# Performance work log

Hardware: AMD Instinct MI355X
Metric: run time of the kernel (lower is better)

The kernel has to match this reference:

```python
import jax, jax.numpy as jnp
import numpy as np
from jax import lax

B, LATENT, SEQ, HID, OUT = 4096, 128, 512, 32, 64


def setup_inputs() -> dict:
    key = jax.random.key(0)
    ks = jax.random.split(key, 9)
    s = 1.0 / np.sqrt(HID)  # PyTorch-style init scale
    f32 = jnp.float32
    return {
        "z": jax.random.normal(ks[0], (B, LATENT), f32),
        "init_W": jax.random.uniform(ks[1], (HID, LATENT), f32, -s, s),
        "init_b": jax.random.uniform(ks[2], (HID,), f32, -s, s),
        "W_ih": jax.random.uniform(ks[3], (4 * HID, HID), f32, -s, s),
        "W_hh": jax.random.uniform(ks[4], (4 * HID, HID), f32, -s, s),
        "b_ih": jax.random.uniform(ks[5], (4 * HID,), f32, -s, s),
        "b_hh": jax.random.uniform(ks[6], (4 * HID,), f32, -s, s),
        "out_W": jax.random.uniform(ks[7], (OUT, HID), f32, -s, s),
        "out_b": jax.random.uniform(ks[8], (OUT,), f32, -s, s),
    }


def reference(z, init_W, init_b, W_ih, W_hh, b_ih, b_hh, out_W, out_b):
    # init_fc: z -> h0 (num_layers=1); cell starts at zero
    h0 = z @ init_W.T + init_b  # [B, H]
    c0 = jnp.zeros_like(h0)

    # x_in is all zeros, so the input-to-hidden term is a constant bias;
    # compute it once (keeps W_ih in the graph, matmul with zeros == 0).
    x_zero = jnp.zeros((z.shape[0], W_ih.shape[1]), z.dtype)
    gate_const = x_zero @ W_ih.T + b_ih + b_hh  # [B, 4H]

    def step(carry, _):
        h, c = carry
        gates = h @ W_hh.T + gate_const  # [B, 4H], PyTorch gate order i,f,g,o
        i, f, g, o = jnp.split(gates, 4, axis=-1)
        i = jax.nn.sigmoid(i)
        f = jax.nn.sigmoid(f)
        g = jnp.tanh(g)
        o = jax.nn.sigmoid(o)
        c = f * c + i * g
        h = o * jnp.tanh(c)
        return (h, c), h

    _, hs = lax.scan(step, (h0, c0), None, length=SEQ)  # [T, B, H]
    out = jnp.transpose(hs, (1, 0, 2))  # [B, T, H] (batch_first)
    y = out @ out_W.T + out_b  # [B, T, OUT]
    return y
```

## Files before the change

### kernel.cpp

```cpp
#include <hip/hip_runtime.h>


#define B_SZ   4096
#define LATENT 128
#define SEQ    512
#define HID    32
#define OUT_N  64
#define ROWS   16
#define LSW    40
#define HXW    10

typedef _Float16 f16x8 __attribute__((ext_vector_type(8)));
typedef _Float16 f16x4 __attribute__((ext_vector_type(4)));
typedef float    f32x4 __attribute__((ext_vector_type(4)));

__device__ __forceinline__ float fexp2(float x) { return __builtin_amdgcn_exp2f(x); }
__device__ __forceinline__ float frcp(float x)  { return __builtin_amdgcn_rcpf(x); }
__device__ __forceinline__ void lds_barrier() {
    asm volatile("s_waitcnt lgkmcnt(0)\n\ts_barrier" ::: "memory");
}

__global__ __launch_bounds__(512)
void lstm_tr11(const float* __restrict__ z,
               const float* __restrict__ init_W,
               const float* __restrict__ init_b,
               const float* __restrict__ W_hh,
               const float* __restrict__ b_ih,
               const float* __restrict__ b_hh,
               const float* __restrict__ out_W,
               const float* __restrict__ out_b,
               float* __restrict__ y)
{
    __shared__ __align__(16) _Float16 hst[ROWS * LSW];
    __shared__ __align__(16) unsigned short hx2[2][64][HXW];

    const int tid  = threadIdx.x;
    const int w    = tid >> 6;
    const int lane = tid & 63;
    const int n_   = lane & 15;
    const int kb   = lane >> 4;
    const int jj   = w & 1;
    const int r_   = w >> 1;
    const int rbase = blockIdx.x * ROWS;

    const float NL2E  = -1.44269504088896341f;
    const float P2L2E =  2.88539008177792681f;

    f16x8 wf1;
    f32x4 bacc1;
    {
        const int arow = 32 * (n_ & 3) + 16 * jj + 4 * (n_ >> 2) + r_;
        const float asc = ((n_ & 3) == 2) ? P2L2E : NL2E;
        const float* wrow = W_hh + (size_t)arow * HID;
#pragma unroll
        for (int rr = 0; rr < 4; rr++) {
            wf1[rr]     = (_Float16)(asc * wrow[4 * kb + rr]);
            wf1[4 + rr] = (_Float16)(asc * wrow[16 + 4 * kb + rr]);
        }
#pragma unroll
        for (int r = 0; r < 4; r++) {
            const int G = 32 * r + 16 * jj + 4 * kb + r_;
            const float bsc = (r == 2) ? P2L2E : NL2E;
            bacc1[r] = bsc * (b_ih[G] + b_hh[G]);
        }
    }

    f16x8 owf;
    f32x4 oacc;
    {
        const int p = r_;
        const float* row = out_W + (size_t)(16 * p + n_) * HID;
#pragma unroll
        for (int rr = 0; rr < 4; rr++) {
            owf[rr]     = (_Float16)row[4 * kb + rr];
            owf[4 + rr] = (_Float16)row[4 * kb + 16 + rr];
        }
#pragma unroll
        for (int r = 0; r < 4; r++) oacc[r] = out_b[16 * p + 4 * kb + r];
    }

    {
        int m = tid >> 5, j = tid & 31;
        const float4* zp = (const float4*)(z + (size_t)(rbase + m) * LATENT);
        const float4* wp = (const float4*)(init_W + (size_t)j * LATENT);
        float acc = init_b[j];
#pragma unroll
        for (int k = 0; k < LATENT / 4; k++) {
            float4 a4 = zp[k], b4 = wp[k];
            acc = fmaf(a4.x, b4.x, acc); acc = fmaf(a4.y, b4.y, acc);
            acc = fmaf(a4.z, b4.z, acc); acc = fmaf(a4.w, b4.w, acc);
        }
        hst[m * LSW + j] = (_Float16)acc;
    }
    __syncthreads();

    f16x8 a;
    {
        f16x4 lo = *(const f16x4*)&hst[n_ * LSW + 4 * kb];
        f16x4 hi = *(const f16x4*)&hst[n_ * LSW + 4 * kb + 16];
#pragma unroll
        for (int r = 0; r < 4; r++) { a[r] = lo[r]; a[4 + r] = hi[r]; }
    }

    float cs = 0.f;

    float* yb = y + (size_t)(rbase + n_) * SEQ * OUT_N + 16 * r_ + 4 * kb;

    for (int t = 0; t < SEQ; t += 4) {
#pragma unroll
        for (int u = 0; u < 4; u++) {
            const int par = u & 1;
            f32x4 acc = __builtin_amdgcn_mfma_f32_16x16x32_f16(wf1, a, bacc1, 0, 0, 0);

            if (jj == par) {
                f32x4 py = __builtin_amdgcn_mfma_f32_16x16x32_f16(owf, a, oacc, 0, 0, 0);
                if (t + u) *(f32x4*)(yb + (size_t)(t + u - 1) * OUT_N) = py;
            }

            {
                float gi = frcp(1.f + fexp2(acc[0]));
                float gf = frcp(1.f + fexp2(acc[1]));
                float rg = frcp(1.f + fexp2(acc[2]));
                float go = frcp(1.f + fexp2(acc[3]));
                float g2 = fmaf(-2.f * P2L2E, rg, P2L2E);
                float csn = fmaf(gf, cs, gi * g2);
                cs = csn;
                float rt = frcp(1.f + fexp2(csn));
                float hh = fmaf(-2.f * go, rt, go);
                union { _Float16 h; unsigned short u16; } cv;
                cv.h = (_Float16)hh;
                hx2[par][lane][4 * jj + r_] = cv.u16;
            }
            lds_barrier();

            {
                union { unsigned int u[4]; f16x8 v; } ua;
                const unsigned int* rp = (const unsigned int*)&hx2[par][lane][0];
                ua.u[0] = rp[0]; ua.u[1] = rp[1]; ua.u[2] = rp[2]; ua.u[3] = rp[3];
                a = ua.v;
            }
        }
    }

    if (jj == 0) {
        f32x4 py = __builtin_amdgcn_mfma_f32_16x16x32_f16(owf, a, oacc, 0, 0, 0);
        *(f32x4*)(yb + (size_t)(SEQ - 1) * OUT_N) = py;
    }
}

extern "C" void kernel_launch(void* const* d_in, const int* in_sizes, int n_in,
                              void* d_out, int out_size, void* d_ws, size_t ws_size,
                              hipStream_t stream) {
    const float* z      = (const float*)d_in[0];
    const float* init_W = (const float*)d_in[1];
    const float* init_b = (const float*)d_in[2];
    const float* W_hh   = (const float*)d_in[4];
    const float* b_ih   = (const float*)d_in[5];
    const float* b_hh   = (const float*)d_in[6];
    const float* out_W  = (const float*)d_in[7];
    const float* out_b  = (const float*)d_in[8];
    float* yout = (float*)d_out;

    lstm_tr11<<<B_SZ / ROWS, 512, 0, stream>>>(z, init_W, init_b, W_hh, b_ih, b_hh,
                                               out_W, out_b, yout);
}
```

Before: 583.5 us.

## Software-pipeline LSTM step: barrier first, lag output projection, fuse gate reciprocals

Each step is reordered so the barrier and LDS read of the new hidden state come first. The output projection then runs on the previous step's hidden state, lagging stores by two steps, which takes it off the recurrence's critical path. All waves now compute the projection and store a subset of rows instead of alternating by parity. The input and candidate gate reciprocals are merged into a single rcp of a product, which saves one transcendental per step but risks overflow when the exponentials grow large. This adds a prologue that moves h0 into the ping-pong buffer and a two-step epilogue.

```diff
diff --git a/kernel.cpp b/kernel.cpp
--- a/kernel.cpp
+++ b/kernel.cpp
@@ -21,7 +21,7 @@
 }
 
 __global__ __launch_bounds__(512)
-void lstm_tr11(const float* __restrict__ z,
+void lstm_sp15(const float* __restrict__ z,
                const float* __restrict__ init_W,
                const float* __restrict__ init_b,
                const float* __restrict__ W_hh,
@@ -32,7 +32,7 @@
                float* __restrict__ y)
 {
     __shared__ __align__(16) _Float16 hst[ROWS * LSW];
-    __shared__ __align__(16) unsigned short hx2[2][64][HXW];
+    __shared__ __align__(4) unsigned short hx[2][64][HXW];
 
     const int tid  = threadIdx.x;
     const int w    = tid >> 6;
@@ -94,57 +94,77 @@
     }
     __syncthreads();
 
+    {
+        union { _Float16 h; unsigned short u16; } cv;
+        cv.h = hst[n_ * LSW + 4 * kb + 16 * jj + r_];
+        hx[0][lane][4 * jj + r_] = cv.u16;
+    }
+    __syncthreads();
+
     f16x8 a;
-    {
-        f16x4 lo = *(const f16x4*)&hst[n_ * LSW + 4 * kb];
-        f16x4 hi = *(const f16x4*)&hst[n_ * LSW + 4 * kb + 16];
 #pragma unroll
-        for (int r = 0; r < 4; r++) { a[r] = lo[r]; a[4 + r] = hi[r]; }
-    }
+    for (int r = 0; r < 8; r++) a[r] = (_Float16)0.f;
 
     float cs = 0.f;
+    const bool vst = ((n_ >> 3) == jj);
 
     float* yb = y + (size_t)(rbase + n_) * SEQ * OUT_N + 16 * r_ + 4 * kb;
 
     for (int t = 0; t < SEQ; t += 4) {
 #pragma unroll
         for (int u = 0; u < 4; u++) {
-            const int par = u & 1;
-            f32x4 acc = __builtin_amdgcn_mfma_f32_16x16x32_f16(wf1, a, bacc1, 0, 0, 0);
+            const int tu = t + u;
+            lds_barrier();
 
-            if (jj == par) {
+            const unsigned* rp = (const unsigned*)&hx[u & 1][lane][0];
+            unsigned t0 = rp[0], t1 = rp[1], t2 = rp[2], t3 = rp[3];
+
+            {
                 f32x4 py = __builtin_amdgcn_mfma_f32_16x16x32_f16(owf, a, oacc, 0, 0, 0);
-                if (t + u) *(f32x4*)(yb + (size_t)(t + u - 1) * OUT_N) = py;
+                if (vst && tu >= 2)
+                    *(f32x4*)(yb + (size_t)(tu - 2) * OUT_N) = py;
             }
 
             {
-                float gi = frcp(1.f + fexp2(acc[0]));
-                float gf = frcp(1.f + fexp2(acc[1]));
-                float rg = frcp(1.f + fexp2(acc[2]));
-                float go = frcp(1.f + fexp2(acc[3]));
-                float g2 = fmaf(-2.f * P2L2E, rg, P2L2E);
-                float csn = fmaf(gf, cs, gi * g2);
+                union { unsigned u4[4]; f16x8 v; } ua;
+                ua.u4[0] = t0; ua.u4[1] = t1; ua.u4[2] = t2; ua.u4[3] = t3;
+                a = ua.v;
+            }
+
+            f32x4 acc = __builtin_amdgcn_mfma_f32_16x16x32_f16(wf1, a, bacc1, 0, 0, 0);
+
+            {
+                float Fi  = fexp2(acc[0]);
+                float Eg  = fexp2(acc[2]);
+                float den = (1.f + Fi) * (1.f + Eg);
+                float rig = frcp(den);
+                float tg  = fmaf(P2L2E, Eg, -P2L2E);
+                float ig  = tg * rig;
+                float gf  = frcp(1.f + fexp2(acc[1]));
+                float csn = fmaf(gf, cs, ig);
                 cs = csn;
-                float rt = frcp(1.f + fexp2(csn));
-                float hh = fmaf(-2.f * go, rt, go);
+                float go  = frcp(1.f + fexp2(acc[3]));
+                float rt  = frcp(1.f + fexp2(csn));
+                float hh  = fmaf(-2.f * go, rt, go);
                 union { _Float16 h; unsigned short u16; } cv;
                 cv.h = (_Float16)hh;
-                hx2[par][lane][4 * jj + r_] = cv.u16;
-            }
-            lds_barrier();
-
-            {
-                union { unsigned int u[4]; f16x8 v; } ua;
-                const unsigned int* rp = (const unsigned int*)&hx2[par][lane][0];
-                ua.u[0] = rp[0]; ua.u[1] = rp[1]; ua.u[2] = rp[2]; ua.u[3] = rp[3];
-                a = ua.v;
+                hx[(u & 1) ^ 1][lane][4 * jj + r_] = cv.u16;
             }
         }
     }
 
-    if (jj == 0) {
+    {
         f32x4 py = __builtin_amdgcn_mfma_f32_16x16x32_f16(owf, a, oacc, 0, 0, 0);
-        *(f32x4*)(yb + (size_t)(SEQ - 1) * OUT_N) = py;
+        if (vst) *(f32x4*)(yb + (size_t)(SEQ - 2) * OUT_N) = py;
+    }
+    lds_barrier();
+    {
+        union { unsigned u4[4]; f16x8 v; } ua;
+        const unsigned* rp = (const unsigned*)&hx[0][lane][0];
+        ua.u4[0] = rp[0]; ua.u4[1] = rp[1]; ua.u4[2] = rp[2]; ua.u4[3] = rp[3];
+        a = ua.v;
+        f32x4 py = __builtin_amdgcn_mfma_f32_16x16x32_f16(owf, a, oacc, 0, 0, 0);
+        if (vst) *(f32x4*)(yb + (size_t)(SEQ - 1) * OUT_N) = py;
     }
 }
 
@@ -161,6 +181,6 @@
     const float* out_b  = (const float*)d_in[8];
     float* yout = (float*)d_out;
 
-    lstm_tr11<<<B_SZ / ROWS, 512, 0, stream>>>(z, init_W, init_b, W_hh, b_ih, b_hh,
+    lstm_sp15<<<B_SZ / ROWS, 512, 0, stream>>>(z, init_W, init_b, W_hh, b_ih, b_hh,
                                                out_W, out_b, yout);
 }
```

New measurement: 590.2 us. No clear change (+1.1%).
